# Performance work log

Hardware: AMD Instinct MI355X
Metric: run time of the kernel (lower is better)

Reference implementation:

```python
import jax, jax.numpy as jnp
import numpy as np

B, DIM, HID = 16384, 512, 256
DT, N_STEPS = 0.1, 3


def setup_inputs() -> dict:
    key = jax.random.key(0)
    ks = jax.random.split(key, 5)
    z = jax.random.normal(ks[0], (B, DIM), dtype=jnp.float32)
    # HNN energy MLP: 2*DIM -> HID -> HID -> 1 (tanh activations)
    s1 = 1.0 / np.sqrt(2 * DIM)
    s2 = 1.0 / np.sqrt(HID)
    W1 = jax.random.normal(ks[1], (2 * DIM, HID), dtype=jnp.float32) * s1
    b1 = jnp.zeros((HID,), dtype=jnp.float32)
    W2 = jax.random.normal(ks[2], (HID, HID), dtype=jnp.float32) * s2
    b2 = jnp.zeros((HID,), dtype=jnp.float32)
    W3 = jax.random.normal(ks[3], (HID, 1), dtype=jnp.float32) * s2
    b3 = jnp.zeros((1,), dtype=jnp.float32)
    return {"z": z, "W1": W1, "b1": b1, "W2": W2, "b2": b2, "W3": W3, "b3": b3}


def reference(z, W1, b1, W2, b2, W3, b3):
    d = z.shape[-1]
    dt = jnp.float32(DT)

    def H_sum(zp):  # total Hamiltonian over the batch -> scalar
        h = jnp.tanh(zp @ W1 + b1)
        h = jnp.tanh(h @ W2 + b2)
        return jnp.sum(h @ W3 + b3)

    gradH = jax.grad(H_sum)  # [B, 2d]: (dH/dq, dH/dp) per sample

    def leapfrog(zp):
        q, p = zp[:, :d], zp[:, d:]
        # half-step momentum: dp/dt = -dH/dq
        g = gradH(jnp.concatenate([q, p], axis=-1))
        p = p - 0.5 * dt * g[:, :d]
        # full-step position: dq/dt = dH/dp
        g = gradH(jnp.concatenate([q, p], axis=-1))
        q = q + dt * g[:, d:]
        # half-step momentum
        g = gradH(jnp.concatenate([q, p], axis=-1))
        p = p - 0.5 * dt * g[:, :d]
        return jnp.concatenate([q, p], axis=-1)

    zp = jnp.concatenate([z, jnp.zeros_like(z)], axis=-1)  # phase space [B, 2d]
    for _ in range(N_STEPS):  # fixed small unroll (n_steps=3)
        zp = leapfrog(zp)
    return zp[:, :d]
```

## Files before the change

### kernel.cpp

```cpp
#include <hip/hip_runtime.h>
#include <math.h>

#define DT 0.1f

typedef __attribute__((ext_vector_type(4)))  short short4v;
typedef __attribute__((ext_vector_type(8)))  short short8;
typedef __attribute__((ext_vector_type(16))) float f32x16;

__device__ __forceinline__ short f2bf(float x) {
    unsigned int u = __float_as_uint(x);
    unsigned int r = (u + 0x7fffu + ((u >> 16) & 1u)) >> 16;
    return (short)r;
}
__device__ __forceinline__ float bf2f(short s) {
    return __uint_as_float(((unsigned int)(unsigned short)s) << 16);
}
__device__ __forceinline__ float tanh_fast(float x) {
    float e = __expf(x + x);
    float r = __builtin_amdgcn_rcpf(e + 1.f);
    return __builtin_fmaf(-2.f, r, 1.f);
}
__device__ __forceinline__ unsigned cvt_pk_bf16(float a, float b) {
    unsigned r;
    asm("v_cvt_pk_bf16_f32 %0, %1, %2" : "=v"(r) : "v"(a), "v"(b));
    return r;
}
__device__ __forceinline__ short8 ldg8(const short8* p) {
    short8 r;
    asm volatile("global_load_dwordx4 %0, %1, off" : "=v"(r) : "v"(p));
    return r;
}

__device__ __forceinline__ void pack32_body(const float* __restrict__ W,
                                            short* __restrict__ out,
                                            int K, int N, int idx, bool trans)
{
    int j = idx & 7, lane = (idx >> 3) & 63, rest = idx >> 9;
    int KT = K >> 4;
    int kt = rest % KT, nt = rest / KT;
    int k = kt * 16 + (lane >> 5) * 8 + j;
    int n = nt * 32 + (lane & 31);
    out[idx] = f2bf(trans ? W[n * K + k] : W[k * N + n]);
}

__global__ __launch_bounds__(256)
void prep(const float* __restrict__ W1, const float* __restrict__ W2,
          const float* __restrict__ z,
          short* __restrict__ PBSq, short* __restrict__ PBSp,
          short* __restrict__ PB2, short* __restrict__ PB2T,
          short* __restrict__ PB1q, short* __restrict__ PB1Tp,
          short* __restrict__ zpA)
{
    __shared__ short zb[32 * 520];
    const int tid = threadIdx.x;
    const int b = blockIdx.x;

    if (b < 512) {
        const int n = tid;
        float s[8];
#pragma unroll
        for (int i = 0; i < 8; ++i) s[i] = 0.f;
        int k; float coef; short* dst;
        if (b < 256) {
            k = b; coef = -0.5f * DT; dst = PBSq;
            for (int c = 0; c < 512; c += 8) {
#pragma unroll
                for (int i = 0; i < 8; ++i)
                    s[i] = __builtin_fmaf(W1[(c + i) * 256 + k],
                                          W1[(512 + c + i) * 256 + n], s[i]);
            }
        } else {
            k = b - 256; coef = DT; dst = PBSp;
            for (int c = 0; c < 512; c += 8) {
#pragma unroll
                for (int i = 0; i < 8; ++i)
                    s[i] = __builtin_fmaf(W1[(512 + c + i) * 256 + k],
                                          W1[(c + i) * 256 + n], s[i]);
            }
        }
        float v = coef * (((s[0] + s[1]) + (s[2] + s[3])) +
                          ((s[4] + s[5]) + (s[6] + s[7])));
        int kt = k >> 4, r = k & 15;
        int lane = (r >> 3) * 32 + (n & 31), nt = n >> 5;
        dst[(((nt * 16 + kt) * 64 + lane) << 3) + (r & 7)] = f2bf(v);
    } else if (b < 768) {
        pack32_body(W2, PB2, 256, 256, (b - 512) * 256 + tid, false);
    } else if (b < 1024) {
        pack32_body(W2, PB2T, 256, 256, (b - 768) * 256 + tid, true);
    } else if (b < 1536) {
        pack32_body(W1, PB1q, 512, 256, (b - 1024) * 256 + tid, false);
    } else if (b < 2048) {
        pack32_body(W1 + 512 * 256, PB1Tp, 256, 512, (b - 1536) * 256 + tid, true);
    } else {
        const int bx = b - 2048;
#pragma unroll
        for (int j = 0; j < 16; ++j) {
            int lin = j * 256 + tid;
            int r = lin >> 7, c4 = lin & 127;
            float4 v = ((const float4*)z)[(size_t)(bx * 32 + r) * 128 + c4];
            uint2 pk;
            pk.x = cvt_pk_bf16(v.x, v.y);
            pk.y = cvt_pk_bf16(v.z, v.w);
            *(uint2*)&zb[r * 520 + c4 * 4] = pk;
        }
        __syncthreads();
        const int lane = tid & 63, w = tid >> 6;
        const int m = lane & 31, lh = lane >> 5;
#pragma unroll
        for (int j = 0; j < 8; ++j) {
            int kt = w * 8 + j;
            short8 f = *(const short8*)&zb[m * 520 + kt * 16 + lh * 8];
            *(short8*)(zpA + (((size_t)bx * 32 + kt) * 64 + lane) * 8) = f;
        }
    }
}

__device__ __forceinline__ short8 lds_frag(const short* Ac, int kt, int mt2,
                                           int l31, int lh, int rot)
{
    int nt_s = kt >> 1;
    int po = (((kt & 1) * 2 + lh) * 4 + rot) & 15;
    int base = ((nt_s * 2 + mt2) * 64 + l31) * 16 + po;
    short4v x = *(const short4v*)&Ac[base];
    short4v y = *(const short4v*)&Ac[base + 512];
    short8 r;
    r[0] = x.x; r[1] = x.y; r[2] = x.z; r[3] = x.w;
    r[4] = y.x; r[5] = y.y; r[6] = y.z; r[7] = y.w;
    return r;
}
__device__ __forceinline__ void store_tile(short* Ac, int nt, int mt2, int lane,
                                           int rot, const f32x16 v)
{
    int base = ((nt * 2 + mt2) * 64 + lane) * 16;
#pragma unroll
    for (int c = 0; c < 4; ++c) {
        uint2 pk;
        pk.x = cvt_pk_bf16(v[4 * c + 0], v[4 * c + 1]);
        pk.y = cvt_pk_bf16(v[4 * c + 2], v[4 * c + 3]);
        *(uint2*)&Ac[base + ((4 * c + rot) & 15)] = pk;
    }
}

__device__ __forceinline__ void gemm_nt(const short* Ac, int l31, int lh, int rot,
                                        const short8* __restrict__ Bf,
                                        f32x16& acc0, f32x16& acc1)
{
    asm volatile("s_waitcnt vmcnt(0)" ::: "memory");
    short8 pb[8];
#pragma unroll
    for (int k = 0; k < 8; ++k) pb[k] = ldg8(Bf + k * 64);
    short8 pa0 = lds_frag(Ac, 0, 0, l31, lh, rot);
    short8 pa1 = lds_frag(Ac, 0, 1, l31, lh, rot);
#pragma unroll
    for (int kt = 0; kt < 16; ++kt) {
        const int N = (15 - kt) < 7 ? (15 - kt) : 7;
        asm volatile("s_waitcnt vmcnt(%1)" : "+v"(pb[kt & 7]) : "i"(N));
        short8 cb = pb[kt & 7];
        if (kt + 8 < 16) pb[kt & 7] = ldg8(Bf + (kt + 8) * 64);
        short8 ca0 = pa0, ca1 = pa1;
        if (kt + 1 < 16) {
            pa0 = lds_frag(Ac, kt + 1, 0, l31, lh, rot);
            pa1 = lds_frag(Ac, kt + 1, 1, l31, lh, rot);
        }
        acc0 = __builtin_amdgcn_mfma_f32_32x32x16_bf16(ca0, cb, acc0, 0, 0, 0);
        acc1 = __builtin_amdgcn_mfma_f32_32x32x16_bf16(ca1, cb, acc1, 0, 0, 0);
    }
}

__global__ __launch_bounds__(512, 1)
void mega(const short* __restrict__ zpA,
          const short* __restrict__ PB1q,
          const short* __restrict__ PB2,
          const short* __restrict__ PB2T,
          const short* __restrict__ PBSq,
          const short* __restrict__ PBSp,
          const float* __restrict__ b1,
          const float* __restrict__ b2,
          const float* __restrict__ W3,
          const short* __restrict__ PB1Tp,
          const float* __restrict__ z,
          float* __restrict__ out)
{
    __shared__ alignas(16) short smem[49152];
    short* h1_c = smem;
    short* da2_c = smem + 16384;
    short* da1_c = smem + 32768;

    const int tid = threadIdx.x;
    const int lane = tid & 63, w = tid >> 6;
    const int l31 = lane & 31, lh = lane >> 5;
    const int rot = ((l31 >> 2) & 3) * 4;
    const int bx = blockIdx.x;

    const int col = w * 32 + l31;
    const float b1v = b1[col], b2v = b2[col], w3v = W3[col];

    const short8* BfPB2  = (const short8*)PB2  + ((size_t)w * 16) * 64 + lane;
    const short8* BfPB2T = (const short8*)PB2T + ((size_t)w * 16) * 64 + lane;
    const short8* BfSq   = (const short8*)PBSq + ((size_t)w * 16) * 64 + lane;
    const short8* BfSp   = (const short8*)PBSp + ((size_t)w * 16) * 64 + lane;

    f32x16 A1[2];  A1[0] = 0.f; A1[1] = 0.f;
    f32x16 dsum[2]; dsum[0] = 0.f; dsum[1] = 0.f;

    {
        const short8* Af0 = (const short8*)zpA + ((size_t)(bx * 2 + 0) * 32) * 64 + lane;
        const short8* Af1 = (const short8*)zpA + ((size_t)(bx * 2 + 1) * 32) * 64 + lane;
        const short8* Bf  = (const short8*)PB1q + ((size_t)w * 32) * 64 + lane;
        short8 pa0[2], pa1[2], pb[4];
#pragma unroll
        for (int k = 0; k < 2; ++k) { pa0[k] = Af0[k * 64]; pa1[k] = Af1[k * 64]; }
#pragma unroll
        for (int k = 0; k < 4; ++k) pb[k] = Bf[k * 64];
#pragma unroll
        for (int kt = 0; kt < 32; ++kt) {
            short8 ca0 = pa0[kt & 1], ca1 = pa1[kt & 1], cb = pb[kt & 3];
            if (kt + 2 < 32) {
                pa0[kt & 1] = Af0[(kt + 2) * 64];
                pa1[kt & 1] = Af1[(kt + 2) * 64];
            }
            if (kt + 4 < 32) pb[kt & 3] = Bf[(kt + 4) * 64];
            A1[0] = __builtin_amdgcn_mfma_f32_32x32x16_bf16(ca0, cb, A1[0], 0, 0, 0);
            A1[1] = __builtin_amdgcn_mfma_f32_32x32x16_bf16(ca1, cb, A1[1], 0, 0, 0);
        }
    }

    for (int it = 0; it < 8; ++it) {
        const bool isq = ((it % 3) == 1);

#pragma unroll
        for (int t = 0; t < 2; ++t) {
            f32x16 hv;
#pragma unroll
            for (int r = 0; r < 16; ++r) hv[r] = tanh_fast(A1[t][r] + b1v);
            store_tile(h1_c, w, t, lane, rot, hv);
        }
        __syncthreads();

        {
            f32x16 t0 = 0.f, t1 = 0.f;
            gemm_nt(h1_c, l31, lh, rot, BfPB2, t0, t1);
#pragma unroll
            for (int t = 0; t < 2; ++t) {
                f32x16& tt = t ? t1 : t0;
                f32x16 d;
#pragma unroll
                for (int r = 0; r < 16; ++r) {
                    float ta = tanh_fast(tt[r] + b2v);
                    d[r] = w3v * (1.f - ta * ta);
                }
                store_tile(da2_c, w, t, lane, rot, d);
            }
        }
        __syncthreads();

        {
            f32x16 t0 = 0.f, t1 = 0.f;
            gemm_nt(da2_c, l31, lh, rot, BfPB2T, t0, t1);
#pragma unroll
            for (int t = 0; t < 2; ++t) {
                f32x16& tt = t ? t1 : t0;
                f32x16 d;
                const int basei = ((w * 2 + t) * 64 + lane) * 16;
#pragma unroll
                for (int c = 0; c < 4; ++c) {
                    short4v h4 = *(const short4v*)&h1_c[basei + ((4 * c + rot) & 15)];
                    float h0 = bf2f(h4.x), h1f = bf2f(h4.y);
                    float h2 = bf2f(h4.z), h3 = bf2f(h4.w);
                    d[4 * c + 0] = tt[4 * c + 0] * (1.f - h0 * h0);
                    d[4 * c + 1] = tt[4 * c + 1] * (1.f - h1f * h1f);
                    d[4 * c + 2] = tt[4 * c + 2] * (1.f - h2 * h2);
                    d[4 * c + 3] = tt[4 * c + 3] * (1.f - h3 * h3);
                }
                if (isq) dsum[t] += d;
                store_tile(da1_c, w, t, lane, rot, d);
            }
        }
        __syncthreads();

        if (it < 7) {
            gemm_nt(da1_c, l31, lh, rot, isq ? BfSp : BfSq, A1[0], A1[1]);
        }
    }

    store_tile(h1_c, w, 0, lane, rot, dsum[0]);
    store_tile(h1_c, w, 1, lane, rot, dsum[1]);
    __syncthreads();

    const int mt = w >> 2;
    const int nq = w & 3;
    {
        const short8* Bf0 = (const short8*)PB1Tp + (size_t)(nq * 4 + 0) * 16 * 64 + lane;
        const short8* Bf1 = (const short8*)PB1Tp + (size_t)(nq * 4 + 1) * 16 * 64 + lane;
        const short8* Bf2 = (const short8*)PB1Tp + (size_t)(nq * 4 + 2) * 16 * 64 + lane;
        const short8* Bf3 = (const short8*)PB1Tp + (size_t)(nq * 4 + 3) * 16 * 64 + lane;
        f32x16 acc4[4];
#pragma unroll
        for (int t = 0; t < 4; ++t) acc4[t] = 0.f;
        short8 br[2][4];
#pragma unroll
        for (int k = 0; k < 2; ++k) {
            br[k][0] = Bf0[k * 64]; br[k][1] = Bf1[k * 64];
            br[k][2] = Bf2[k * 64]; br[k][3] = Bf3[k * 64];
        }
#pragma unroll
        for (int kt = 0; kt < 16; ++kt) {
            short8 a = lds_frag(h1_c, kt, mt, l31, lh, rot);
            short8 bb[4];
#pragma unroll
            for (int t = 0; t < 4; ++t) bb[t] = br[kt & 1][t];
            if (kt + 2 < 16) {
                br[kt & 1][0] = Bf0[(kt + 2) * 64];
                br[kt & 1][1] = Bf1[(kt + 2) * 64];
                br[kt & 1][2] = Bf2[(kt + 2) * 64];
                br[kt & 1][3] = Bf3[(kt + 2) * 64];
            }
#pragma unroll
            for (int t = 0; t < 4; ++t)
                acc4[t] = __builtin_amdgcn_mfma_f32_32x32x16_bf16(a, bb[t], acc4[t], 0, 0, 0);
        }
        __syncthreads();

        float* Ct = (float*)smem;
#pragma unroll
        for (int p = 0; p < 2; ++p) {
            if (mt == p) {
#pragma unroll
                for (int t = 0; t < 4; ++t) {
                    const int c = (nq * 4 + t) * 32 + l31;
#pragma unroll
                    for (int r = 0; r < 16; ++r) {
                        int row = (r & 3) + 8 * (r >> 2) + 4 * lh;
                        Ct[row * 512 + c] = acc4[t][r];
                    }
                }
            }
            __syncthreads();
#pragma unroll
            for (int j = 0; j < 8; ++j) {
                int lin = j * 512 + tid;
                int r = lin >> 7, c4 = lin & 127;
                size_t gi = (size_t)(bx * 64 + p * 32 + r) * 128 + c4;
                float4 zv = ((const float4*)z)[gi];
                float4 cv = *(const float4*)&Ct[r * 512 + c4 * 4];
                float4 ov;
                ov.x = zv.x + DT * cv.x; ov.y = zv.y + DT * cv.y;
                ov.z = zv.z + DT * cv.z; ov.w = zv.w + DT * cv.w;
                ((float4*)out)[gi] = ov;
            }
            __syncthreads();
        }
    }
}

extern "C" void kernel_launch(void* const* d_in, const int* in_sizes, int n_in,
                              void* d_out, int out_size, void* d_ws, size_t ws_size,
                              hipStream_t stream)
{
    const float* z  = (const float*)d_in[0];
    const float* W1 = (const float*)d_in[1];
    const float* b1 = (const float*)d_in[2];
    const float* W2 = (const float*)d_in[3];
    const float* b2 = (const float*)d_in[4];
    const float* W3 = (const float*)d_in[5];
    float* out = (float*)d_out;

    short* PB2   = (short*)d_ws;
    short* PB2T  = PB2   + 65536;
    short* PBSq  = PB2T  + 65536;
    short* PBSp  = PBSq  + 65536;
    short* PB1q  = PBSp  + 65536;
    short* PB1Tp = PB1q  + 131072;
    short* zpA   = PB1Tp + 131072;

    prep<<<2560, 256, 0, stream>>>(W1, W2, z, PBSq, PBSp, PB2, PB2T,
                                   PB1q, PB1Tp, zpA);
    mega<<<256, 512, 0, stream>>>(zpA, PB1q, PB2, PB2T, PBSq, PBSp,
                                  b1, b2, W3, PB1Tp, z, out);
}
```

Before: 195.6 us.

## Split row tiles into two halves and overlap VALU epilogues with MFMA GEMMs

The two 32-row M-tiles per block are now processed as a software pipeline. Each GEMM handles one half-tile while the tanh/derivative epilogue for the other half is interleaved into the MFMA loop through a lambda. The aim is to hide transcendental and elementwise VALU work behind matrix-core execution instead of running them serially between barriers. In exchange there are twice as many GEMM calls and barriers per iteration, each with half the MFMA work, plus extra B-fragment reloads from global/L2 and more complex register live ranges.

```diff
diff --git a/kernel.cpp b/kernel.cpp
--- a/kernel.cpp
+++ b/kernel.cpp
@@ -141,29 +141,55 @@
     }
 }
 
-__device__ __forceinline__ void gemm_nt(const short* Ac, int l31, int lh, int rot,
-                                        const short8* __restrict__ Bf,
-                                        f32x16& acc0, f32x16& acc1)
+__device__ __forceinline__ short8 lds_frag32(const short* Ac, int kt,
+                                             int l31, int lh, int rot)
+{
+    int nt_s = kt >> 1;
+    int po = (((kt & 1) * 2 + lh) * 4 + rot) & 15;
+    int base = (nt_s * 64 + l31) * 16 + po;
+    short4v x = *(const short4v*)&Ac[base];
+    short4v y = *(const short4v*)&Ac[base + 512];
+    short8 r;
+    r[0] = x.x; r[1] = x.y; r[2] = x.z; r[3] = x.w;
+    r[4] = y.x; r[5] = y.y; r[6] = y.z; r[7] = y.w;
+    return r;
+}
+__device__ __forceinline__ void store_tile32(short* Ac, int nt, int lane,
+                                             int rot, const f32x16 v)
+{
+    int base = (nt * 64 + lane) * 16;
+#pragma unroll
+    for (int c = 0; c < 4; ++c) {
+        uint2 pk;
+        pk.x = cvt_pk_bf16(v[4 * c + 0], v[4 * c + 1]);
+        pk.y = cvt_pk_bf16(v[4 * c + 2], v[4 * c + 3]);
+        *(uint2*)&Ac[base + ((4 * c + rot) & 15)] = pk;
+    }
+}
+
+template <typename F>
+__device__ __forceinline__ void gemm_f(const short* Ac, int l31, int lh, int rot,
+                                       const short8* __restrict__ Bf,
+                                       f32x16& acc, F valu)
 {
     asm volatile("s_waitcnt vmcnt(0)" ::: "memory");
     short8 pb[8];
 #pragma unroll
     for (int k = 0; k < 8; ++k) pb[k] = ldg8(Bf + k * 64);
-    short8 pa0 = lds_frag(Ac, 0, 0, l31, lh, rot);
-    short8 pa1 = lds_frag(Ac, 0, 1, l31, lh, rot);
+    short8 pa0 = lds_frag32(Ac, 0, l31, lh, rot);
+    short8 pa1 = lds_frag32(Ac, 1, l31, lh, rot);
+    valu(0); valu(1); valu(2); valu(3);
 #pragma unroll
     for (int kt = 0; kt < 16; ++kt) {
+        if (kt < 12) valu(kt + 4);
         const int N = (15 - kt) < 7 ? (15 - kt) : 7;
         asm volatile("s_waitcnt vmcnt(%1)" : "+v"(pb[kt & 7]) : "i"(N));
         short8 cb = pb[kt & 7];
         if (kt + 8 < 16) pb[kt & 7] = ldg8(Bf + (kt + 8) * 64);
-        short8 ca0 = pa0, ca1 = pa1;
-        if (kt + 1 < 16) {
-            pa0 = lds_frag(Ac, kt + 1, 0, l31, lh, rot);
-            pa1 = lds_frag(Ac, kt + 1, 1, l31, lh, rot);
-        }
-        acc0 = __builtin_amdgcn_mfma_f32_32x32x16_bf16(ca0, cb, acc0, 0, 0, 0);
-        acc1 = __builtin_amdgcn_mfma_f32_32x32x16_bf16(ca1, cb, acc1, 0, 0, 0);
+        short8 ca = pa0;
+        pa0 = pa1;
+        if (kt + 2 < 16) pa1 = lds_frag32(Ac, kt + 2, l31, lh, rot);
+        acc = __builtin_amdgcn_mfma_f32_32x32x16_bf16(ca, cb, acc, 0, 0, 0);
     }
 }
 
@@ -181,10 +207,13 @@
           const float* __restrict__ z,
           float* __restrict__ out)
 {
-    __shared__ alignas(16) short smem[49152];
-    short* h1_c = smem;
-    short* da2_c = smem + 16384;
-    short* da1_c = smem + 32768;
+    __shared__ alignas(16) short smem[32768];
+    short* h1_a  = smem;
+    short* h1_b  = smem + 4096;
+    short* da2_a = smem + 8192;
+    short* da2_b = smem + 12288;
+    short* da1_a = smem + 16384;
+    short* da1_b = smem + 20480;
 
     const int tid = threadIdx.x;
     const int lane = tid & 63, w = tid >> 6;
@@ -194,14 +223,15 @@
 
     const int col = w * 32 + l31;
     const float b1v = b1[col], b2v = b2[col], w3v = W3[col];
+    const int basei = (w * 64 + lane) * 16;
 
     const short8* BfPB2  = (const short8*)PB2  + ((size_t)w * 16) * 64 + lane;
     const short8* BfPB2T = (const short8*)PB2T + ((size_t)w * 16) * 64 + lane;
     const short8* BfSq   = (const short8*)PBSq + ((size_t)w * 16) * 64 + lane;
     const short8* BfSp   = (const short8*)PBSp + ((size_t)w * 16) * 64 + lane;
 
-    f32x16 A1[2];  A1[0] = 0.f; A1[1] = 0.f;
-    f32x16 dsum[2]; dsum[0] = 0.f; dsum[1] = 0.f;
+    f32x16 A1a = 0.f, A1b = 0.f;
+    f32x16 dsa = 0.f, dsb = 0.f;
 
     {
         const short8* Af0 = (const short8*)zpA + ((size_t)(bx * 2 + 0) * 32) * 64 + lane;
@@ -220,71 +250,93 @@
                 pa1[kt & 1] = Af1[(kt + 2) * 64];
             }
             if (kt + 4 < 32) pb[kt & 3] = Bf[(kt + 4) * 64];
-            A1[0] = __builtin_amdgcn_mfma_f32_32x32x16_bf16(ca0, cb, A1[0], 0, 0, 0);
-            A1[1] = __builtin_amdgcn_mfma_f32_32x32x16_bf16(ca1, cb, A1[1], 0, 0, 0);
-        }
-    }
+            A1a = __builtin_amdgcn_mfma_f32_32x32x16_bf16(ca0, cb, A1a, 0, 0, 0);
+            A1b = __builtin_amdgcn_mfma_f32_32x32x16_bf16(ca1, cb, A1b, 0, 0, 0);
+        }
+    }
+
+    {
+        f32x16 d;
+#pragma unroll
+        for (int r = 0; r < 16; ++r) d[r] = tanh_fast(A1a[r] + b1v);
+        store_tile32(h1_a, w, lane, rot, d);
+    }
+    __syncthreads();
+
+    f32x16 u_b = 0.f;
 
     for (int it = 0; it < 8; ++it) {
         const bool isq = ((it % 3) == 1);
-
-#pragma unroll
-        for (int t = 0; t < 2; ++t) {
-            f32x16 hv;
-#pragma unroll
-            for (int r = 0; r < 16; ++r) hv[r] = tanh_fast(A1[t][r] + b1v);
-            store_tile(h1_c, w, t, lane, rot, hv);
-        }
-        __syncthreads();
-
-        {
-            f32x16 t0 = 0.f, t1 = 0.f;
-            gemm_nt(h1_c, l31, lh, rot, BfPB2, t0, t1);
-#pragma unroll
-            for (int t = 0; t < 2; ++t) {
-                f32x16& tt = t ? t1 : t0;
-                f32x16 d;
-#pragma unroll
-                for (int r = 0; r < 16; ++r) {
-                    float ta = tanh_fast(tt[r] + b2v);
-                    d[r] = w3v * (1.f - ta * ta);
-                }
-                store_tile(da2_c, w, t, lane, rot, d);
-            }
-        }
-        __syncthreads();
-
-        {
-            f32x16 t0 = 0.f, t1 = 0.f;
-            gemm_nt(da2_c, l31, lh, rot, BfPB2T, t0, t1);
-#pragma unroll
-            for (int t = 0; t < 2; ++t) {
-                f32x16& tt = t ? t1 : t0;
-                f32x16 d;
-                const int basei = ((w * 2 + t) * 64 + lane) * 16;
-#pragma unroll
-                for (int c = 0; c < 4; ++c) {
-                    short4v h4 = *(const short4v*)&h1_c[basei + ((4 * c + rot) & 15)];
-                    float h0 = bf2f(h4.x), h1f = bf2f(h4.y);
-                    float h2 = bf2f(h4.z), h3 = bf2f(h4.w);
-                    d[4 * c + 0] = tt[4 * c + 0] * (1.f - h0 * h0);
-                    d[4 * c + 1] = tt[4 * c + 1] * (1.f - h1f * h1f);
-                    d[4 * c + 2] = tt[4 * c + 2] * (1.f - h2 * h2);
-                    d[4 * c + 3] = tt[4 * c + 3] * (1.f - h3 * h3);
-                }
-                if (isq) dsum[t] += d;
-                store_tile(da1_c, w, t, lane, rot, d);
-            }
-        }
+        const short8* BfS = isq ? BfSp : BfSq;
+        f32x16 t_a = 0.f, t_b = 0.f, u_a = 0.f;
+        f32x16 d;
+        short4v h4;
+
+        gemm_f(h1_a, l31, lh, rot, BfPB2, t_a, [&](int kt) {
+            d[kt] = tanh_fast(A1b[kt] + b1v);
+        });
+        store_tile32(h1_b, w, lane, rot, d);
+        __syncthreads();
+
+        gemm_f(h1_b, l31, lh, rot, BfPB2, t_b, [&](int kt) {
+            float ta = tanh_fast(t_a[kt] + b2v);
+            d[kt] = w3v * (1.f - ta * ta);
+        });
+        store_tile32(da2_a, w, lane, rot, d);
+        __syncthreads();
+
+        gemm_f(da2_a, l31, lh, rot, BfPB2T, u_a, [&](int kt) {
+            float ta = tanh_fast(t_b[kt] + b2v);
+            d[kt] = w3v * (1.f - ta * ta);
+        });
+        store_tile32(da2_b, w, lane, rot, d);
+        __syncthreads();
+
+        u_b = 0.f;
+        gemm_f(da2_b, l31, lh, rot, BfPB2T, u_b, [&](int kt) {
+            if ((kt & 3) == 0)
+                h4 = *(const short4v*)&h1_a[basei + ((kt + rot) & 15)];
+            float h = bf2f((kt & 3) == 0 ? h4.x : (kt & 3) == 1 ? h4.y
+                         : (kt & 3) == 2 ? h4.z : h4.w);
+            d[kt] = u_a[kt] * (1.f - h * h);
+        });
+        if (isq) dsa += d;
+        store_tile32(da1_a, w, lane, rot, d);
         __syncthreads();
 
         if (it < 7) {
-            gemm_nt(da1_c, l31, lh, rot, isq ? BfSp : BfSq, A1[0], A1[1]);
-        }
-    }
-
-    store_tile(h1_c, w, 0, lane, rot, dsum[0]);
-    store_tile(h1_c, w, 1, lane, rot, dsum[1]);
+            gemm_f(da1_a, l31, lh, rot, BfS, A1a, [&](int kt) {
+                if ((kt & 3) == 0)
+                    h4 = *(const short4v*)&h1_b[basei + ((kt + rot) & 15)];
+                float h = bf2f((kt & 3) == 0 ? h4.x : (kt & 3) == 1 ? h4.y
+                             : (kt & 3) == 2 ? h4.z : h4.w);
+                d[kt] = u_b[kt] * (1.f - h * h);
+            });
+            if (isq) dsb += d;
+            store_tile32(da1_b, w, lane, rot, d);
+            __syncthreads();
+
+            gemm_f(da1_b, l31, lh, rot, BfS, A1b, [&](int kt) {
+                d[kt] = tanh_fast(A1a[kt] + b1v);
+            });
+            store_tile32(h1_a, w, lane, rot, d);
+            __syncthreads();
+        } else {
+#pragma unroll
+            for (int kt = 0; kt < 16; ++kt) {
+                if ((kt & 3) == 0)
+                    h4 = *(const short4v*)&h1_b[basei + ((kt + rot) & 15)];
+                float h = bf2f((kt & 3) == 0 ? h4.x : (kt & 3) == 1 ? h4.y
+                             : (kt & 3) == 2 ? h4.z : h4.w);
+                d[kt] = u_b[kt] * (1.f - h * h);
+            }
+            dsb += d;
+            __syncthreads();
+        }
+    }
+
+    store_tile(smem, w, 0, lane, rot, dsa);
+    store_tile(smem, w, 1, lane, rot, dsb);
     __syncthreads();
 
     const int mt = w >> 2;
@@ -305,7 +357,7 @@
         }
 #pragma unroll
         for (int kt = 0; kt < 16; ++kt) {
-            short8 a = lds_frag(h1_c, kt, mt, l31, lh, rot);
+            short8 a = lds_frag(smem, kt, mt, l31, lh, rot);
             short8 bb[4];
 #pragma unroll
             for (int t = 0; t < 4; ++t) bb[t] = br[kt & 1][t];
```

Measured after the change: 231.6 us. 1.18x slower.
